# Optimization experiments

Hardware: AMD Instinct MI355X
Metric: run time of the kernel (lower is better)

## Reference

```python
import jax, jax.numpy as jnp
import numpy as np

B, M, N, HID, H, P = 16, 1024, 1024, 512, 8, 2
DH = HID // H


def setup_inputs() -> dict:
    key = jax.random.key(0)
    k1, k2, k3, k4 = jax.random.split(key, 4)
    X = jax.random.normal(k1, (B, M, HID), dtype=jnp.float32)
    Y = jax.random.normal(k2, (B, N, HID), dtype=jnp.float32)
    # learned pad prefixes (kaiming-uniform in torch; any init is fine for a numerics baseline)
    bound = np.sqrt(1.0 / HID)
    pad_x = jax.random.uniform(k3, (P, HID), dtype=jnp.float32, minval=-bound, maxval=bound)
    pad_y = jax.random.uniform(k4, (P, HID), dtype=jnp.float32, minval=-bound, maxval=bound)
    return {"X": X, "Y": Y, "pad_x": pad_x, "pad_y": pad_y}


def _project(T, pad):
    # prepend learned pad rows, split into heads -> [B, H, L+P, DH]
    b = T.shape[0]
    T = jnp.concatenate([jnp.broadcast_to(pad[None], (b, P, HID)), T], axis=1)
    return T.reshape(b, T.shape[1], H, DH).transpose(0, 2, 1, 3)


def reference(X, Y, pad_x, pad_y):
    Xp = _project(X, pad_x)  # [B,H,Mp,DH], query=key=value
    Yp = _project(Y, pad_y)  # [B,H,Np,DH]
    # shared similarity matrix (no 1/sqrt(d) scaling in the original)
    sim = jnp.einsum('bhmd,bhnd->bhmn', Xp, Yp)  # [B,H,Mp,Np]
    # masks in the original are all-ones (pad rows + torch.ones), so masked_fill is a no-op
    attn_X_by_Y = jax.nn.softmax(sim, axis=2)  # softmax over Mp (rows)
    attn_Y_by_X = jax.nn.softmax(sim, axis=3)  # softmax over Np (cols)
    # X attends in Y: attn^T @ X_value -> [B,H,Np,DH]
    X_in_Y = jnp.einsum('bhmn,bhmd->bhnd', attn_X_by_Y, Xp)[:, :, P:, :]
    X_in_Y = X_in_Y.transpose(0, 2, 1, 3).reshape(X.shape[0], -1, HID)  # [B,N,HID]
    # Y attends in X: attn @ Y_value -> [B,H,Mp,DH]
    Y_in_X = jnp.einsum('bhmn,bhnd->bhmd', attn_Y_by_X, Yp)[:, :, P:, :]
    Y_in_X = Y_in_X.transpose(0, 2, 1, 3).reshape(Y.shape[0], -1, HID)  # [B,M,HID]
    return X_in_Y, Y_in_X
```

## Files before the change

### kernel.cpp

```cpp
#include <hip/hip_runtime.h>
#include <hip/hip_bf16.h>
#include <stdint.h>

typedef _Float16 f16x8_t  __attribute__((ext_vector_type(8)));
typedef float    f32x16_t __attribute__((ext_vector_type(16)));
typedef short    s16x8_t  __attribute__((ext_vector_type(8)));
typedef unsigned uint2v   __attribute__((ext_vector_type(2)));
typedef unsigned int u32;

#define MFMA32 __builtin_amdgcn_mfma_f32_32x32x16_f16

#if __has_builtin(__builtin_amdgcn_exp2f)
#define EXP2(x) __builtin_amdgcn_exp2f(x)
#else
#define EXP2(x) exp2f(x)
#endif

__device__ __forceinline__ u32 PKRTZ(float a, float b) {
    return __builtin_bit_cast(u32, __builtin_amdgcn_cvt_pkrtz(a, b));
}

__device__ __forceinline__ void PLSWAP(u32& a, u32& b) {
#if __has_builtin(__builtin_amdgcn_permlane32_swap)
    uint2v r = __builtin_amdgcn_permlane32_swap(a, b, false, false);
    a = r[0]; b = r[1];
#else
    u32 pa = (u32)__shfl_xor((int)a, 32);
    u32 pb = (u32)__shfl_xor((int)b, 32);
    const int hi_ = (int)((threadIdx.x & 63) >> 5);
    u32 na = hi_ ? pb : a;
    u32 nb = hi_ ? b  : pa;
    a = na; b = nb;
#endif
}
__device__ __forceinline__ float swap_add(float v) {
    u32 a = __builtin_bit_cast(u32, v), b = a;
    PLSWAP(a, b);
    return __builtin_bit_cast(float, a) + __builtin_bit_cast(float, b);
}
__device__ __forceinline__ float swap_max(float v) {
    u32 a = __builtin_bit_cast(u32, v), b = a;
    PLSWAP(a, b);
    return fmaxf(__builtin_bit_cast(float, a), __builtin_bit_cast(float, b));
}

constexpr int Bb   = 16;
constexpr int HIDc = 512;
constexpr int SEQc = 1024;

constexpr int QT = 128;
constexpr int KT = 64;
constexpr int NTILES = SEQc / KT;

constexpr float LOG2E_F = 1.4426950408889634f;
constexpr float DTHR    = 11.5f;

constexpr int ROWB       = 144;
constexpr int VT_OFF     = 64 * ROWB;
constexpr int BUF_STRIDE = 2 * VT_OFF;
constexpr int LDS_TOTAL  = 2 * BUF_STRIDE;

__global__ __launch_bounds__(256, 4)
void xattn_kernel(const float* __restrict__ X, const float* __restrict__ Y,
                  const float* __restrict__ padx, const float* __restrict__ pady,
                  float* __restrict__ out)
{
    __shared__ __align__(16) unsigned char pool[LDS_TOTAL];

    const int tid  = threadIdx.x;
    const int w    = tid >> 6;
    const int lane = tid & 63;
    const int l31  = lane & 31;
    const int hi   = lane >> 5;

    const unsigned hid = blockIdx.x + gridDim.x * (blockIdx.y + gridDim.y * blockIdx.z);
    const unsigned lid = (hid & 7u) * 256u + (hid >> 3);
    const int qt   = lid & 7;
    const int bh   = (lid >> 3) & 127;
    const int pass = lid >> 10;
    const int b    = bh >> 3;
    const int h    = bh & 7;

    const float* Qp   = pass == 0 ? X : Y;
    const float* KVp  = pass == 0 ? Y : X;
    const float* padp = pass == 0 ? pady : padx;
    float* outp = out + (pass == 0 ? (size_t)Bb * SEQc * HIDc : (size_t)0);

    const float* qrow = Qp + ((size_t)b * SEQc + qt * QT + w * 32 + l31) * HIDc + h * 64;
    f16x8_t qf[4];
#pragma unroll
    for (int ds = 0; ds < 4; ++ds) {
        const float* src = qrow + ds * 16 + hi * 8;
        float4 a = *(const float4*)src;
        float4 c = *(const float4*)(src + 4);
        uint4 uu = {PKRTZ(a.x * LOG2E_F, a.y * LOG2E_F), PKRTZ(a.z * LOG2E_F, a.w * LOG2E_F),
                    PKRTZ(c.x * LOG2E_F, c.y * LOG2E_F), PKRTZ(c.z * LOG2E_F, c.w * LOG2E_F)};
        qf[ds] = __builtin_bit_cast(f16x8_t, uu);
    }

    const float* padh = padp + h * 64;
    float s0 = 0.f, s1 = 0.f;
#pragma unroll
    for (int ds = 0; ds < 4; ++ds)
#pragma unroll
        for (int j = 0; j < 8; ++j) {
            float qv = (float)qf[ds][j];
            int d = ds * 16 + hi * 8 + j;
            s0 += qv * padh[d];
            s1 += qv * padh[HIDc + d];
        }
    s0 = swap_add(s0);
    s1 = swap_add(s1);
    float mr = fmaxf(s0, s1);
    float e0 = EXP2(s0 - mr), e1 = EXP2(s1 - mr);
    float lr = e0 + e1;

    f32x16_t Oacc[2];
#pragma unroll
    for (int db = 0; db < 2; ++db)
#pragma unroll
        for (int r = 0; r < 16; ++r) {
            int d = db * 32 + (r & 3) + 8 * (r >> 2) + 4 * hi;
            Oacc[db][r] = e0 * padh[d] + e1 * padh[HIDc + d];
        }

    const unsigned kkey = (unsigned)(((l31 >> 3) & 3) << 4);
    const unsigned vkey = (unsigned)((l31 >> 3) << 4);
    const unsigned rowb = (unsigned)(l31 * ROWB);
    unsigned kcol[4], vcol[4];
#pragma unroll
    for (int s = 0; s < 4; ++s) {
        kcol[s] = (unsigned)((s * 32 + hi * 16) ^ kkey);
        vcol[s] = (unsigned)(VT_OFF + ((s * 32 + hi * 16) ^ vkey));
    }

    const int tr = tid >> 3, tc = tid & 7;
    const float* ksrc = KVp + ((size_t)b * SEQc + 2 * tr) * HIDc + h * 64 + tc * 8;
    const unsigned kw  = (unsigned)((2 * tr) * ROWB + ((tc * 16) ^ ((((2 * tr) >> 3) & 3) << 4)));
    const unsigned vtw = (unsigned)(VT_OFF + (tc * 8) * ROWB + ((4 * tr) ^ (tc << 4)));

    auto loadtile = [&](int idx, float4& a0, float4& a1, float4& c0, float4& c1) {
        const float* srow = ksrc + (size_t)idx * KT * HIDc;
        a0 = *(const float4*)srow;          a1 = *(const float4*)(srow + 4);
        c0 = *(const float4*)(srow + HIDc); c1 = *(const float4*)(srow + HIDc + 4);
    };
    auto stage_write = [&](int bo, const float4& a0, const float4& a1,
                           const float4& c0, const float4& c1) {
        uint4 k0 = {PKRTZ(a0.x, a0.y), PKRTZ(a0.z, a0.w), PKRTZ(a1.x, a1.y), PKRTZ(a1.z, a1.w)};
        uint4 k1 = {PKRTZ(c0.x, c0.y), PKRTZ(c0.z, c0.w), PKRTZ(c1.x, c1.y), PKRTZ(c1.z, c1.w)};
        *(uint4*)(pool + bo + kw) = k0;
        *(uint4*)(pool + bo + kw + ROWB) = k1;
        float fa[8] = {a0.x, a0.y, a0.z, a0.w, a1.x, a1.y, a1.z, a1.w};
        float fc[8] = {c0.x, c0.y, c0.z, c0.w, c1.x, c1.y, c1.z, c1.w};
#pragma unroll
        for (int j = 0; j < 8; ++j)
            *(u32*)(pool + bo + vtw + j * ROWB) = PKRTZ(fa[j], fc[j]);
    };

    auto compute = [&](int bo) {
        f32x16_t sa[2];
#pragma unroll
        for (int nb = 0; nb < 2; ++nb)
#pragma unroll
            for (int r = 0; r < 16; ++r) sa[nb][r] = 0.f;
        __builtin_amdgcn_s_setprio(1);
#pragma unroll
        for (int ds = 0; ds < 4; ++ds) {
            s16x8_t k0 = *(const s16x8_t*)(pool + bo + rowb + kcol[ds]);
            s16x8_t k1 = *(const s16x8_t*)(pool + bo + rowb + kcol[ds] + 32 * ROWB);
            sa[0] = MFMA32(__builtin_bit_cast(f16x8_t, k0), qf[ds], sa[0], 0, 0, 0);
            sa[1] = MFMA32(__builtin_bit_cast(f16x8_t, k1), qf[ds], sa[1], 0, 0, 0);
        }
        __builtin_amdgcn_s_setprio(0);

        float pm = sa[0][0];
#pragma unroll
        for (int nb = 0; nb < 2; ++nb)
#pragma unroll
            for (int r = 0; r < 16; ++r) pm = fmaxf(pm, sa[nb][r]);
        pm = swap_max(pm);
        if (!__all(pm <= mr + DTHR)) {
            float mn = fmaxf(mr, pm);
            float corr = EXP2(mr - mn);
            mr = mn;
            lr *= corr;
#pragma unroll
            for (int db = 0; db < 2; ++db)
#pragma unroll
                for (int r = 0; r < 16; ++r) Oacc[db][r] *= corr;
        }

        float ps = 0.f;
        __builtin_amdgcn_s_setprio(1);
#pragma unroll
        for (int nb = 0; nb < 2; ++nb)
#pragma unroll
            for (int ksl = 0; ksl < 2; ++ksl) {
                float x0 = EXP2(sa[nb][8 * ksl + 0] - mr);
                float x1 = EXP2(sa[nb][8 * ksl + 1] - mr);
                float x2 = EXP2(sa[nb][8 * ksl + 2] - mr);
                float x3 = EXP2(sa[nb][8 * ksl + 3] - mr);
                float x4 = EXP2(sa[nb][8 * ksl + 4] - mr);
                float x5 = EXP2(sa[nb][8 * ksl + 5] - mr);
                float x6 = EXP2(sa[nb][8 * ksl + 6] - mr);
                float x7 = EXP2(sa[nb][8 * ksl + 7] - mr);
                ps += ((x0 + x1) + (x2 + x3)) + ((x4 + x5) + (x6 + x7));
                u32 w0 = PKRTZ(x0, x1);
                u32 w1 = PKRTZ(x2, x3);
                u32 w2 = PKRTZ(x4, x5);
                u32 w3 = PKRTZ(x6, x7);
                PLSWAP(w0, w2);
                PLSWAP(w1, w3);
                uint4 pu = {w0, w1, w2, w3};
                f16x8_t pfrag = __builtin_bit_cast(f16x8_t, pu);
                const int ks = nb * 2 + ksl;
                s16x8_t v0 = *(const s16x8_t*)(pool + bo + rowb + vcol[ks]);
                s16x8_t v1 = *(const s16x8_t*)(pool + bo + rowb + (vcol[ks] ^ 0x40u) + 32 * ROWB);
                Oacc[0] = MFMA32(__builtin_bit_cast(f16x8_t, v0), pfrag, Oacc[0], 0, 0, 0);
                Oacc[1] = MFMA32(__builtin_bit_cast(f16x8_t, v1), pfrag, Oacc[1], 0, 0, 0);
            }
        __builtin_amdgcn_s_setprio(0);
        lr += swap_add(ps);
    };

    {
        float4 a0, a1, c0, c1;
        loadtile(0, a0, a1, c0, c1);
        stage_write(0, a0, a1, c0, c1);
    }
    __syncthreads();
    for (int kt = 0; kt < NTILES; kt += 2) {
        {
            compute(0);
            float4 a0, a1, c0, c1;
            loadtile(kt + 1, a0, a1, c0, c1);
            stage_write(BUF_STRIDE, a0, a1, c0, c1);
            __syncthreads();
        }
        {
            compute(BUF_STRIDE);
            if (kt + 2 < NTILES) {
                float4 a0, a1, c0, c1;
                loadtile(kt + 2, a0, a1, c0, c1);
                stage_write(0, a0, a1, c0, c1);
            }
            __syncthreads();
        }
    }

    {
        const float inv = 1.0f / lr;
        float* fp = (float*)pool;
#pragma unroll
        for (int db = 0; db < 2; ++db)
#pragma unroll
            for (int r = 0; r < 16; ++r) {
                int d = db * 32 + (r & 3) + 8 * (r >> 2) + 4 * hi;
                fp[(w * 32 + l31) * 68 + d] = Oacc[db][r] * inv;
            }
    }
    __syncthreads();
    {
        const int row = tid >> 1, ch = tid & 1;
        const float* srcp = (const float*)pool + row * 68 + ch * 32;
        float* dst = outp + ((size_t)b * SEQc + qt * QT + row) * HIDc + h * 64 + ch * 32;
#pragma unroll
        for (int k = 0; k < 8; ++k)
            *(float4*)(dst + k * 4) = *(const float4*)(srcp + k * 4);
    }
}

extern "C" void kernel_launch(void* const* d_in, const int* in_sizes, int n_in,
                              void* d_out, int out_size, void* d_ws, size_t ws_size,
                              hipStream_t stream) {
    const float* X    = (const float*)d_in[0];
    const float* Y    = (const float*)d_in[1];
    const float* padx = (const float*)d_in[2];
    const float* pady = (const float*)d_in[3];
    float* out = (float*)d_out;
    (void)in_sizes; (void)n_in; (void)out_size; (void)d_ws; (void)ws_size;

    dim3 grid(SEQc / QT, Bb * 8, 2);
    hipLaunchKernelGGL(xattn_kernel, grid, dim3(256), 0, stream, X, Y, padx, pady, out);
}
```

Measured before the change: 106.1 us.

## Double query tile to 256 rows with 512-thread blocks sharing K/V staging

Each block now handles 256 query rows with 8 waves instead of 128 rows with 4, so every K/V tile staged in LDS is reused by twice as many waves. The per-thread share of loading and converting the tile is halved, and the output epilogue is split into two halves through the same LDS buffer. This cuts global K/V traffic and staging work per query row, but halves the grid to 1024 blocks and requests 4 blocks of 512 threads per CU in the launch bounds, which tightens register limits and may reduce occupancy.

```diff
diff --git a/kernel.cpp b/kernel.cpp
--- a/kernel.cpp
+++ b/kernel.cpp
@@ -48,7 +48,7 @@
 constexpr int HIDc = 512;
 constexpr int SEQc = 1024;
 
-constexpr int QT = 128;
+constexpr int QT = 256;
 constexpr int KT = 64;
 constexpr int NTILES = SEQc / KT;
 
@@ -60,7 +60,7 @@
 constexpr int BUF_STRIDE = 2 * VT_OFF;
 constexpr int LDS_TOTAL  = 2 * BUF_STRIDE;
 
-__global__ __launch_bounds__(256, 4)
+__global__ __launch_bounds__(512, 4)
 void xattn_kernel(const float* __restrict__ X, const float* __restrict__ Y,
                   const float* __restrict__ padx, const float* __restrict__ pady,
                   float* __restrict__ out)
@@ -74,10 +74,10 @@
     const int hi   = lane >> 5;
 
     const unsigned hid = blockIdx.x + gridDim.x * (blockIdx.y + gridDim.y * blockIdx.z);
-    const unsigned lid = (hid & 7u) * 256u + (hid >> 3);
-    const int qt   = lid & 7;
-    const int bh   = (lid >> 3) & 127;
-    const int pass = lid >> 10;
+    const unsigned lid = (hid & 7u) * 128u + (hid >> 3);
+    const int qt   = lid & 3;
+    const int bh   = (lid >> 2) & 127;
+    const int pass = lid >> 9;
     const int b    = bh >> 3;
     const int h    = bh & 7;
 
@@ -134,26 +134,25 @@
         vcol[s] = (unsigned)(VT_OFF + ((s * 32 + hi * 16) ^ vkey));
     }
 
-    const int tr = tid >> 3, tc = tid & 7;
-    const float* ksrc = KVp + ((size_t)b * SEQc + 2 * tr) * HIDc + h * 64 + tc * 8;
-    const unsigned kw  = (unsigned)((2 * tr) * ROWB + ((tc * 16) ^ ((((2 * tr) >> 3) & 3) << 4)));
-    const unsigned vtw = (unsigned)(VT_OFF + (tc * 8) * ROWB + ((4 * tr) ^ (tc << 4)));
-
-    auto loadtile = [&](int idx, float4& a0, float4& a1, float4& c0, float4& c1) {
+    const int tr = tid >> 4, tc2 = tid & 15;
+    const float* ksrc = KVp + ((size_t)b * SEQc + 2 * tr) * HIDc + h * 64 + tc2 * 4;
+    const unsigned kw  = (unsigned)((2 * tr) * ROWB + ((tc2 * 8) ^ ((((2 * tr) >> 3) & 3) << 4)));
+    const unsigned vtw = (unsigned)(VT_OFF + (tc2 * 4) * ROWB + ((4 * tr) ^ ((tc2 >> 1) << 4)));
+
+    auto loadtile = [&](int idx, float4& a0, float4& c0) {
         const float* srow = ksrc + (size_t)idx * KT * HIDc;
-        a0 = *(const float4*)srow;          a1 = *(const float4*)(srow + 4);
-        c0 = *(const float4*)(srow + HIDc); c1 = *(const float4*)(srow + HIDc + 4);
+        a0 = *(const float4*)srow;
+        c0 = *(const float4*)(srow + HIDc);
     };
-    auto stage_write = [&](int bo, const float4& a0, const float4& a1,
-                           const float4& c0, const float4& c1) {
-        uint4 k0 = {PKRTZ(a0.x, a0.y), PKRTZ(a0.z, a0.w), PKRTZ(a1.x, a1.y), PKRTZ(a1.z, a1.w)};
-        uint4 k1 = {PKRTZ(c0.x, c0.y), PKRTZ(c0.z, c0.w), PKRTZ(c1.x, c1.y), PKRTZ(c1.z, c1.w)};
-        *(uint4*)(pool + bo + kw) = k0;
-        *(uint4*)(pool + bo + kw + ROWB) = k1;
-        float fa[8] = {a0.x, a0.y, a0.z, a0.w, a1.x, a1.y, a1.z, a1.w};
-        float fc[8] = {c0.x, c0.y, c0.z, c0.w, c1.x, c1.y, c1.z, c1.w};
-#pragma unroll
-        for (int j = 0; j < 8; ++j)
+    auto stage_write = [&](int bo, const float4& a0, const float4& c0) {
+        uint2 k0 = {PKRTZ(a0.x, a0.y), PKRTZ(a0.z, a0.w)};
+        uint2 k1 = {PKRTZ(c0.x, c0.y), PKRTZ(c0.z, c0.w)};
+        *(uint2*)(pool + bo + kw) = k0;
+        *(uint2*)(pool + bo + kw + ROWB) = k1;
+        float fa[4] = {a0.x, a0.y, a0.z, a0.w};
+        float fc[4] = {c0.x, c0.y, c0.z, c0.w};
+#pragma unroll
+        for (int j = 0; j < 4; ++j)
             *(u32*)(pool + bo + vtw + j * ROWB) = PKRTZ(fa[j], fc[j]);
     };
 
@@ -224,48 +223,51 @@
     };
 
     {
-        float4 a0, a1, c0, c1;
-        loadtile(0, a0, a1, c0, c1);
-        stage_write(0, a0, a1, c0, c1);
+        float4 a0, c0;
+        loadtile(0, a0, c0);
+        stage_write(0, a0, c0);
     }
     __syncthreads();
     for (int kt = 0; kt < NTILES; kt += 2) {
         {
             compute(0);
-            float4 a0, a1, c0, c1;
-            loadtile(kt + 1, a0, a1, c0, c1);
-            stage_write(BUF_STRIDE, a0, a1, c0, c1);
+            float4 a0, c0;
+            loadtile(kt + 1, a0, c0);
+            stage_write(BUF_STRIDE, a0, c0);
             __syncthreads();
         }
         {
             compute(BUF_STRIDE);
             if (kt + 2 < NTILES) {
-                float4 a0, a1, c0, c1;
-                loadtile(kt + 2, a0, a1, c0, c1);
-                stage_write(0, a0, a1, c0, c1);
+                float4 a0, c0;
+                loadtile(kt + 2, a0, c0);
+                stage_write(0, a0, c0);
             }
             __syncthreads();
         }
     }
 
-    {
-        const float inv = 1.0f / lr;
-        float* fp = (float*)pool;
-#pragma unroll
-        for (int db = 0; db < 2; ++db)
-#pragma unroll
-            for (int r = 0; r < 16; ++r) {
-                int d = db * 32 + (r & 3) + 8 * (r >> 2) + 4 * hi;
-                fp[(w * 32 + l31) * 68 + d] = Oacc[db][r] * inv;
-            }
-    }
-    __syncthreads();
-    {
-        const int row = tid >> 1, ch = tid & 1;
-        const float* srcp = (const float*)pool + row * 68 + ch * 32;
-        float* dst = outp + ((size_t)b * SEQc + qt * QT + row) * HIDc + h * 64 + ch * 32;
-#pragma unroll
-        for (int k = 0; k < 8; ++k)
+    const float inv = 1.0f / lr;
+    float* fp = (float*)pool;
+#pragma unroll
+    for (int half = 0; half < 2; ++half) {
+        __syncthreads();
+        if ((w >> 2) == half) {
+#pragma unroll
+            for (int db = 0; db < 2; ++db)
+#pragma unroll
+                for (int r = 0; r < 16; ++r) {
+                    int d = db * 32 + (r & 3) + 8 * (r >> 2) + 4 * hi;
+                    fp[((w & 3) * 32 + l31) * 68 + d] = Oacc[db][r] * inv;
+                }
+        }
+        __syncthreads();
+        const int row = tid >> 2, ch = tid & 3;
+        const float* srcp = fp + row * 68 + ch * 16;
+        float* dst = outp + ((size_t)b * SEQc + qt * QT + half * 128 + row) * HIDc
+                     + h * 64 + ch * 16;
+#pragma unroll
+        for (int k = 0; k < 4; ++k)
             *(float4*)(dst + k * 4) = *(const float4*)(srcp + k * 4);
     }
 }
@@ -281,5 +283,5 @@
     (void)in_sizes; (void)n_in; (void)out_size; (void)d_ws; (void)ws_size;
 
     dim3 grid(SEQc / QT, Bb * 8, 2);
-    hipLaunchKernelGGL(xattn_kernel, grid, dim3(256), 0, stream, X, Y, padx, pady, out);
-}
+    hipLaunchKernelGGL(xattn_kernel, grid, dim3(512), 0, stream, X, Y, padx, pady, out);
+}
```

Result: slower. 108.4 us (+2.2%).

## Split key sequence across two wave groups per block and merge softmax partials

Applied to the files above, without the earlier changes.

Doubles the block to 512 threads so two groups of four waves each process half of the key/value sequence for the same 128 query rows, with separate double-buffered LDS regions per half. The partial max, sum and output accumulators of the second half are merged into the first through LDS with online-softmax rescaling before the normalized write-out. This halves the serial key loop per wave and adds parallelism, at the cost of doubled LDS use (which may limit blocks per CU), extra syncs and a merge step.

```diff
diff --git a/kernel.cpp b/kernel.cpp
--- a/kernel.cpp
+++ b/kernel.cpp
@@ -50,17 +50,19 @@
 
 constexpr int QT = 128;
 constexpr int KT = 64;
-constexpr int NTILES = SEQc / KT;
+constexpr int HTILES = 8;
 
 constexpr float LOG2E_F = 1.4426950408889634f;
 constexpr float DTHR    = 11.5f;
-
-constexpr int ROWB       = 144;
-constexpr int VT_OFF     = 64 * ROWB;
-constexpr int BUF_STRIDE = 2 * VT_OFF;
-constexpr int LDS_TOTAL  = 2 * BUF_STRIDE;
-
-__global__ __launch_bounds__(256, 4)
+constexpr float NEG_INF = -1e30f;
+
+constexpr int ROWB        = 144;
+constexpr int VT_OFF      = 64 * ROWB;
+constexpr int BUF_STRIDE  = 2 * VT_OFF;
+constexpr int HALF_STRIDE = 2 * BUF_STRIDE;
+constexpr int LDS_TOTAL   = 2 * HALF_STRIDE;
+
+__global__ __launch_bounds__(512, 4)
 void xattn_kernel(const float* __restrict__ X, const float* __restrict__ Y,
                   const float* __restrict__ padx, const float* __restrict__ pady,
                   float* __restrict__ out)
@@ -69,9 +71,12 @@
 
     const int tid  = threadIdx.x;
     const int w    = tid >> 6;
+    const int wg   = w & 3;
+    const int wh   = w >> 2;
     const int lane = tid & 63;
     const int l31  = lane & 31;
     const int hi   = lane >> 5;
+    const unsigned hoff = (unsigned)(wh * HALF_STRIDE);
 
     const unsigned hid = blockIdx.x + gridDim.x * (blockIdx.y + gridDim.y * blockIdx.z);
     const unsigned lid = (hid & 7u) * 256u + (hid >> 3);
@@ -86,7 +91,7 @@
     const float* padp = pass == 0 ? pady : padx;
     float* outp = out + (pass == 0 ? (size_t)Bb * SEQc * HIDc : (size_t)0);
 
-    const float* qrow = Qp + ((size_t)b * SEQc + qt * QT + w * 32 + l31) * HIDc + h * 64;
+    const float* qrow = Qp + ((size_t)b * SEQc + qt * QT + wg * 32 + l31) * HIDc + h * 64;
     f16x8_t qf[4];
 #pragma unroll
     for (int ds = 0; ds < 4; ++ds) {
@@ -99,30 +104,39 @@
     }
 
     const float* padh = padp + h * 64;
-    float s0 = 0.f, s1 = 0.f;
-#pragma unroll
-    for (int ds = 0; ds < 4; ++ds)
-#pragma unroll
-        for (int j = 0; j < 8; ++j) {
-            float qv = (float)qf[ds][j];
-            int d = ds * 16 + hi * 8 + j;
-            s0 += qv * padh[d];
-            s1 += qv * padh[HIDc + d];
-        }
-    s0 = swap_add(s0);
-    s1 = swap_add(s1);
-    float mr = fmaxf(s0, s1);
-    float e0 = EXP2(s0 - mr), e1 = EXP2(s1 - mr);
-    float lr = e0 + e1;
-
+    float mr, lr;
     f32x16_t Oacc[2];
-#pragma unroll
-    for (int db = 0; db < 2; ++db)
-#pragma unroll
-        for (int r = 0; r < 16; ++r) {
-            int d = db * 32 + (r & 3) + 8 * (r >> 2) + 4 * hi;
-            Oacc[db][r] = e0 * padh[d] + e1 * padh[HIDc + d];
-        }
+    if (wh == 0) {
+        float s0 = 0.f, s1 = 0.f;
+#pragma unroll
+        for (int ds = 0; ds < 4; ++ds)
+#pragma unroll
+            for (int j = 0; j < 8; ++j) {
+                float qv = (float)qf[ds][j];
+                int d = ds * 16 + hi * 8 + j;
+                s0 += qv * padh[d];
+                s1 += qv * padh[HIDc + d];
+            }
+        s0 = swap_add(s0);
+        s1 = swap_add(s1);
+        mr = fmaxf(s0, s1);
+        float e0 = EXP2(s0 - mr), e1 = EXP2(s1 - mr);
+        lr = e0 + e1;
+#pragma unroll
+        for (int db = 0; db < 2; ++db)
+#pragma unroll
+            for (int r = 0; r < 16; ++r) {
+                int d = db * 32 + (r & 3) + 8 * (r >> 2) + 4 * hi;
+                Oacc[db][r] = e0 * padh[d] + e1 * padh[HIDc + d];
+            }
+    } else {
+        mr = NEG_INF;
+        lr = 0.f;
+#pragma unroll
+        for (int db = 0; db < 2; ++db)
+#pragma unroll
+            for (int r = 0; r < 16; ++r) Oacc[db][r] = 0.f;
+    }
 
     const unsigned kkey = (unsigned)(((l31 >> 3) & 3) << 4);
     const unsigned vkey = (unsigned)((l31 >> 3) << 4);
@@ -134,8 +148,9 @@
         vcol[s] = (unsigned)(VT_OFF + ((s * 32 + hi * 16) ^ vkey));
     }
 
-    const int tr = tid >> 3, tc = tid & 7;
-    const float* ksrc = KVp + ((size_t)b * SEQc + 2 * tr) * HIDc + h * 64 + tc * 8;
+    const int tid8 = tid & 255;
+    const int tr = tid8 >> 3, tc = tid8 & 7;
+    const float* ksrc = KVp + ((size_t)b * SEQc + wh * 512 + 2 * tr) * HIDc + h * 64 + tc * 8;
     const unsigned kw  = (unsigned)((2 * tr) * ROWB + ((tc * 16) ^ ((((2 * tr) >> 3) & 3) << 4)));
     const unsigned vtw = (unsigned)(VT_OFF + (tc * 8) * ROWB + ((4 * tr) ^ (tc << 4)));
 
@@ -144,7 +159,7 @@
         a0 = *(const float4*)srow;          a1 = *(const float4*)(srow + 4);
         c0 = *(const float4*)(srow + HIDc); c1 = *(const float4*)(srow + HIDc + 4);
     };
-    auto stage_write = [&](int bo, const float4& a0, const float4& a1,
+    auto stage_write = [&](unsigned bo, const float4& a0, const float4& a1,
                            const float4& c0, const float4& c1) {
         uint4 k0 = {PKRTZ(a0.x, a0.y), PKRTZ(a0.z, a0.w), PKRTZ(a1.x, a1.y), PKRTZ(a1.z, a1.w)};
         uint4 k1 = {PKRTZ(c0.x, c0.y), PKRTZ(c0.z, c0.w), PKRTZ(c1.x, c1.y), PKRTZ(c1.z, c1.w)};
@@ -157,7 +172,7 @@
             *(u32*)(pool + bo + vtw + j * ROWB) = PKRTZ(fa[j], fc[j]);
     };
 
-    auto compute = [&](int bo) {
+    auto compute = [&](unsigned bo) {
         f32x16_t sa[2];
 #pragma unroll
         for (int nb = 0; nb < 2; ++nb)
@@ -226,46 +241,70 @@
     {
         float4 a0, a1, c0, c1;
         loadtile(0, a0, a1, c0, c1);
-        stage_write(0, a0, a1, c0, c1);
+        stage_write(hoff, a0, a1, c0, c1);
     }
     __syncthreads();
-    for (int kt = 0; kt < NTILES; kt += 2) {
+    for (int t = 0; t < HTILES; t += 2) {
         {
-            compute(0);
+            compute(hoff);
             float4 a0, a1, c0, c1;
-            loadtile(kt + 1, a0, a1, c0, c1);
-            stage_write(BUF_STRIDE, a0, a1, c0, c1);
+            loadtile(t + 1, a0, a1, c0, c1);
+            stage_write(hoff + BUF_STRIDE, a0, a1, c0, c1);
             __syncthreads();
         }
         {
-            compute(BUF_STRIDE);
-            if (kt + 2 < NTILES) {
+            compute(hoff + BUF_STRIDE);
+            if (t + 2 < HTILES) {
                 float4 a0, a1, c0, c1;
-                loadtile(kt + 2, a0, a1, c0, c1);
-                stage_write(0, a0, a1, c0, c1);
+                loadtile(t + 2, a0, a1, c0, c1);
+                stage_write(hoff, a0, a1, c0, c1);
             }
             __syncthreads();
         }
     }
 
-    {
-        const float inv = 1.0f / lr;
-        float* fp = (float*)pool;
+    float* mb = (float*)pool + ((size_t)wg * 64 + lane) * 34;
+    if (wh == 1) {
+#pragma unroll
+        for (int db = 0; db < 2; ++db)
+#pragma unroll
+            for (int r = 0; r < 16; ++r) mb[db * 16 + r] = Oacc[db][r];
+        mb[32] = mr;
+        mb[33] = lr;
+    }
+    __syncthreads();
+    float inv = 0.f;
+    if (wh == 0) {
+        float mB = mb[32], lB = mb[33];
+        float m  = fmaxf(mr, mB);
+        float cA = EXP2(mr - m), cB = EXP2(mB - m);
+        float lfull = lr * cA + lB * cB;
+        inv = 1.0f / lfull;
+#pragma unroll
+        for (int db = 0; db < 2; ++db)
+#pragma unroll
+            for (int r = 0; r < 16; ++r)
+                Oacc[db][r] = Oacc[db][r] * cA + mb[db * 16 + r] * cB;
+    }
+    __syncthreads();
+
+    float* fp = (float*)pool;
+    if (wh == 0) {
 #pragma unroll
         for (int db = 0; db < 2; ++db)
 #pragma unroll
             for (int r = 0; r < 16; ++r) {
                 int d = db * 32 + (r & 3) + 8 * (r >> 2) + 4 * hi;
-                fp[(w * 32 + l31) * 68 + d] = Oacc[db][r] * inv;
+                fp[(wg * 32 + l31) * 68 + d] = Oacc[db][r] * inv;
             }
     }
     __syncthreads();
     {
-        const int row = tid >> 1, ch = tid & 1;
-        const float* srcp = (const float*)pool + row * 68 + ch * 32;
-        float* dst = outp + ((size_t)b * SEQc + qt * QT + row) * HIDc + h * 64 + ch * 32;
-#pragma unroll
-        for (int k = 0; k < 8; ++k)
+        const int row = tid >> 2, ch = tid & 3;
+        const float* srcp = fp + row * 68 + ch * 16;
+        float* dst = outp + ((size_t)b * SEQc + qt * QT + row) * HIDc + h * 64 + ch * 16;
+#pragma unroll
+        for (int k = 0; k < 4; ++k)
             *(float4*)(dst + k * 4) = *(const float4*)(srcp + k * 4);
     }
 }
@@ -281,5 +320,5 @@
     (void)in_sizes; (void)n_in; (void)out_size; (void)d_ws; (void)ws_size;
 
     dim3 grid(SEQc / QT, Bb * 8, 2);
-    hipLaunchKernelGGL(xattn_kernel, grid, dim3(256), 0, stream, X, Y, padx, pady, out);
-}
+    hipLaunchKernelGGL(xattn_kernel, grid, dim3(512), 0, stream, X, Y, padx, pady, out);
+}
```

Result: slower. 113.4 us (+6.9%).
